# Kernel tuning notes

Measured on AMD Instinct MI355X. Metric: run time of the kernel, lower is better.

The kernel has to match this reference:

```python
import jax, jax.numpy as jnp
import numpy as np
from jax import lax

N_STEPS = 64  # fixed-step RK4 stands in for torchdiffeq's adaptive dopri5
INPUT_DIM = 64
HIDDEN_DIM = 256
BATCH = 262144


def setup_inputs() -> dict:
    key = jax.random.key(0)
    k_x, k_t, k_w1, k_b1, k_w2, k_b2 = jax.random.split(key, 6)
    x = jax.random.normal(k_x, (BATCH, INPUT_DIM), dtype=jnp.float32)
    t = jax.random.uniform(k_t, (1,), dtype=jnp.float32, minval=0.1, maxval=1.0)
    # torch Linear convention: y = x @ W.T + b
    s1 = 1.0 / np.sqrt(INPUT_DIM)
    s2 = 1.0 / np.sqrt(HIDDEN_DIM)
    W1 = jax.random.uniform(k_w1, (HIDDEN_DIM, INPUT_DIM), jnp.float32, -s1, s1)
    b1 = jax.random.uniform(k_b1, (HIDDEN_DIM,), jnp.float32, -s1, s1)
    W2 = jax.random.uniform(k_w2, (INPUT_DIM, HIDDEN_DIM), jnp.float32, -s2, s2)
    b2 = jax.random.uniform(k_b2, (INPUT_DIM,), jnp.float32, -s2, s2)
    return {"x": x, "t": t, "W1": W1, "b1": b1, "W2": W2, "b2": b2}


def reference(x, t, W1, b1, W2, b2):
    # ODE dynamics: f(y) = Linear2(ELU(Linear1(y))) -- autonomous (no t dependence)
    def f(y):
        h = jax.nn.elu(y @ W1.T + b1)  # [B, H]
        return h @ W2.T + b2           # [B, D]

    t0 = jnp.reshape(t, (-1,))[0]      # t.squeeze(); integrate over [0, t0]
    dt = t0 / N_STEPS

    def step(y, _):
        k1 = f(y)
        k2 = f(y + 0.5 * dt * k1)
        k3 = f(y + 0.5 * dt * k2)
        k4 = f(y + dt * k3)
        y_next = y + (dt / 6.0) * (k1 + 2.0 * k2 + 2.0 * k3 + k4)
        return y_next, None

    y_final, _ = lax.scan(step, x, None, length=N_STEPS)
    return y_final  # out[-1]: state at time t0
```

## Files before the change

### kernel.cpp

```cpp
#include <hip/hip_runtime.h>

#define NSTEP 64

typedef short bf8 __attribute__((ext_vector_type(8)));
typedef float f32x16 __attribute__((ext_vector_type(16)));
typedef float f32x4 __attribute__((ext_vector_type(4)));
typedef float f32x2 __attribute__((ext_vector_type(2)));
typedef unsigned int u32x4 __attribute__((ext_vector_type(4)));
typedef unsigned int u32x2 __attribute__((ext_vector_type(2)));

static __device__ __forceinline__ float asf(unsigned int u){ return __builtin_bit_cast(float, u); }
static __device__ __forceinline__ unsigned int asu(float f){ return __builtin_bit_cast(unsigned int, f); }

#if defined(__has_builtin)
#if __has_builtin(__builtin_amdgcn_cvt_pk_bf16_f32)
#define HAVE_CVT_PK_BF16 1
#endif
#endif
#ifdef HAVE_CVT_PK_BF16
typedef __bf16 bf16x2_t __attribute__((ext_vector_type(2)));
static __device__ __forceinline__ unsigned int pk(float a, float b){
  bf16x2_t r = __builtin_amdgcn_cvt_pk_bf16_f32(a, b);
  return __builtin_bit_cast(unsigned int, r);
}
#else
static __device__ __forceinline__ unsigned int pk(float a, float b){
  unsigned int ua = asu(a); unsigned int ub = asu(b);
  ua += 0x7FFFu + ((ua >> 16) & 1u);
  ub += 0x7FFFu + ((ub >> 16) & 1u);
  return (ua >> 16) | (ub & 0xFFFF0000u);
}
#endif

static __device__ __forceinline__ float bfr(float w){ return asf(pk(w, 0.0f) << 16); }

static __device__ __forceinline__ f32x2 pkfma(f32x2 a, f32x2 b, f32x2 c){
  return __builtin_elementwise_fma(a, b, c);
}

static __device__ __forceinline__ f32x2 pairof(const f32x16& v, int j){
  f32x2 r; r.x = v[2*j]; r.y = v[2*j+1]; return r;
}
static __device__ __forceinline__ void setpair(f32x16& v, int j, f32x2 p){
  v[2*j] = p.x; v[2*j+1] = p.y;
}

static __device__ __forceinline__ bf8 scale_bf8(bf8 w, float s){
  u32x4 u = __builtin_bit_cast(u32x4, w);
  u32x4 r;
  #pragma unroll
  for(int i=0;i<4;i++){
    float lo = asf(u[i] << 16) * s;
    float hi = asf(u[i] & 0xFFFF0000u) * s;
    r[i] = pk(lo, hi);
  }
  return __builtin_bit_cast(bf8, r);
}

#define MFMA16 __builtin_amdgcn_mfma_f32_16x16x32_bf16


#define ELU2(A, H0, H1) { \
  f32x2 q0; q0.x=A[0]; q0.y=A[1]; \
  f32x2 q1; q1.x=A[2]; q1.y=A[3]; \
  f32x2 m0 = __builtin_elementwise_max(q0, Z2); \
  f32x2 n0 = __builtin_elementwise_min(q0, Z2); \
  f32x2 m1 = __builtin_elementwise_max(q1, Z2); \
  f32x2 n1 = __builtin_elementwise_min(q1, Z2); \
  f32x2 e0; e0.x=__builtin_amdgcn_exp2f(n0.x); e0.y=__builtin_amdgcn_exp2f(n0.y); \
  f32x2 e1; e1.x=__builtin_amdgcn_exp2f(n1.x); e1.y=__builtin_amdgcn_exp2f(n1.y); \
  f32x2 h0 = pkfma(m0, LN22, e0); \
  f32x2 h1 = pkfma(m1, LN22, e1); \
  H0 = pk(h0.x, h0.y); H1 = pk(h1.x, h1.y); \
}

__global__ __launch_bounds__(128, 2) void ode_kernel(
    const void* __restrict__ xv,
    const void* __restrict__ tv,
    const void* __restrict__ W1v,
    const void* __restrict__ b1v,
    const void* __restrict__ W2v,
    const void* __restrict__ b2v,
    void* __restrict__ outv)
{
  __shared__ __align__(16) float b1s[256];
  __shared__ __align__(16) float b2s[64];
  __shared__ __align__(16) float xbuf[2][2][1024];

  const int tid = threadIdx.x;
  const int lid = tid & 63;
  const int wv  = tid >> 6;

  const unsigned int* w1u = (const unsigned int*)W1v;
  bool bad = false;
  #pragma unroll
  for(int i=0; i<2; i++){
    unsigned int d = w1u[i*64 + lid];
    unsigned int e0 = (d >> 7)  & 0xFFu;
    unsigned int e1 = (d >> 23) & 0xFFu;
    bad |= (e0 >= 125u) || (e1 >= 125u);
  }
  const bool f32in = (__ballot(bad) != 0ull);

  const float L2E = 1.4426950408889634f;

  if(f32in){
    #pragma unroll
    for(int i=0; i<2; i++) b1s[tid + i*128] = ((const float*)b1v)[tid + i*128] * L2E;
  } else {
    #pragma unroll
    for(int i=0; i<2; i++)
      b1s[tid + i*128] = asf((unsigned int)((const unsigned short*)b1v)[tid + i*128] << 16) * L2E;
  }
  if(tid < 64){
    float ssum = 0.0f;
    if(f32in){
      const float* W2 = (const float*)W2v + tid*256;
      #pragma unroll 4
      for(int k=0; k<64; k++){
        f32x4 w4 = *(const f32x4*)(W2 + k*4);
        ssum += bfr(w4[0]) + bfr(w4[1]) + bfr(w4[2]) + bfr(w4[3]);
      }
    } else {
      const unsigned short* W2 = (const unsigned short*)W2v + tid*256;
      for(int k=0; k<256; k++) ssum += asf((unsigned int)W2[k] << 16);
    }
    float bb = f32in ? ((const float*)b2v)[tid]
                     : asf((unsigned int)((const unsigned short*)b2v)[tid] << 16);
    b2s[tid] = (bb - ssum) * 0.5f;
  }
  __syncthreads();

  const int ln = lid & 15;
  const int g  = lid >> 4;
  const int g4 = g * 4;
  const int rr = blockIdx.x * 16 + ln;

  const float t  = f32in ? ((const float*)tv)[0]
                         : asf((unsigned int)((const unsigned short*)tv)[0] << 16);
  const float dt  = t / (float)NSTEP;
  const float hdt = 0.5f * dt;
  const float gg  = dt * (1.0f/6.0f);
  const f32x2 DT2  = {dt, dt};
  const f32x2 HDT2 = {hdt, hdt};
  const f32x2 TWO2 = {2.0f, 2.0f};
  const f32x2 G2   = {gg, gg};
  const f32x2 LN22 = {0.6931471805599453f, 0.6931471805599453f};
  const f32x2 Z2   = {0.0f, 0.0f};

  bf8 W1f[8][2];
  bf8 W2f[4][4];
  if(f32in){
    const float* W1 = (const float*)W1v;
    const float* W2 = (const float*)W2v;
    #pragma unroll
    for(int mtl=0; mtl<8; mtl++){
      #pragma unroll
      for(int ks=0; ks<2; ks++){
        const float* p = W1 + (wv*128 + mtl*16 + ln)*64 + ks*32 + g4;
        f32x4 a = *(const f32x4*)p;
        f32x4 b = *(const f32x4*)(p + 16);
        u32x4 u;
        u[0]=pk(a[0]*L2E, a[1]*L2E); u[1]=pk(a[2]*L2E, a[3]*L2E);
        u[2]=pk(b[0]*L2E, b[1]*L2E); u[3]=pk(b[2]*L2E, b[3]*L2E);
        W1f[mtl][ks] = __builtin_bit_cast(bf8, u);
      }
    }
    #pragma unroll
    for(int mt=0; mt<4; mt++){
      #pragma unroll
      for(int kt=0; kt<4; kt++){
        const float* p = W2 + (mt*16 + ln)*256 + wv*128 + kt*32 + g4;
        f32x4 a = *(const f32x4*)p;
        f32x4 b = *(const f32x4*)(p + 16);
        u32x4 u; u[0]=pk(a[0],a[1]); u[1]=pk(a[2],a[3]); u[2]=pk(b[0],b[1]); u[3]=pk(b[2],b[3]);
        W2f[mt][kt] = __builtin_bit_cast(bf8, u);
      }
    }
  } else {
    const unsigned short* W1 = (const unsigned short*)W1v;
    const unsigned short* W2 = (const unsigned short*)W2v;
    #pragma unroll
    for(int mtl=0; mtl<8; mtl++){
      #pragma unroll
      for(int ks=0; ks<2; ks++){
        const unsigned short* p = W1 + (wv*128 + mtl*16 + ln)*64 + ks*32 + g4;
        u32x2 lo = *(const u32x2*)p;
        u32x2 hi = *(const u32x2*)(p + 16);
        u32x4 u; u[0]=lo[0]; u[1]=lo[1]; u[2]=hi[0]; u[3]=hi[1];
        W1f[mtl][ks] = scale_bf8(__builtin_bit_cast(bf8, u), L2E);
      }
    }
    #pragma unroll
    for(int mt=0; mt<4; mt++){
      #pragma unroll
      for(int kt=0; kt<4; kt++){
        const unsigned short* p = W2 + (mt*16 + ln)*256 + wv*128 + kt*32 + g4;
        u32x2 lo = *(const u32x2*)p;
        u32x2 hi = *(const u32x2*)(p + 16);
        u32x4 u; u[0]=lo[0]; u[1]=lo[1]; u[2]=hi[0]; u[3]=hi[1];
        W2f[mt][kt] = __builtin_bit_cast(bf8, u);
      }
    }
  }

  f32x16 Y;
  if(f32in){
    const float* x = (const float*)xv;
    #pragma unroll
    for(int mt=0; mt<4; mt++){
      f32x4 v = *(const f32x4*)(x + rr*64 + mt*16 + g4);
      #pragma unroll
      for(int i=0;i<4;i++) Y[4*mt+i] = v[i];
    }
  } else {
    const unsigned short* x = (const unsigned short*)xv;
    #pragma unroll
    for(int mt=0; mt<4; mt++){
      u32x2 v = *(const u32x2*)(x + rr*64 + mt*16 + g4);
      Y[4*mt+0]=asf(v[0]<<16); Y[4*mt+1]=asf(v[0]&0xFFFF0000u);
      Y[4*mt+2]=asf(v[1]<<16); Y[4*mt+3]=asf(v[1]&0xFFFF0000u);
    }
  }

  f32x16 c2;
  #pragma unroll
  for(int i=0;i<16;i++) c2[i]=0.0f;

  #define CHUNK(KT) { \
    f32x4 a0 = *(const f32x4*)&b1s[wv*128 + (2*KT)*16 + g4]; \
    f32x4 a1 = *(const f32x4*)&b1s[wv*128 + (2*KT+1)*16 + g4]; \
    a0 = MFMA16(W1f[2*KT  ][0], zf0, a0, 0,0,0); \
    a0 = MFMA16(W1f[2*KT  ][1], zf1, a0, 0,0,0); \
    a1 = MFMA16(W1f[2*KT+1][0], zf0, a1, 0,0,0); \
    a1 = MFMA16(W1f[2*KT+1][1], zf1, a1, 0,0,0); \
    unsigned int H00,H01,H10,H11; \
    ELU2(a0, H00, H01) \
    ELU2(a1, H10, H11) \
    u32x4 hu; hu[0]=H00; hu[1]=H01; hu[2]=H10; hu[3]=H11; \
    bf8 hf = __builtin_bit_cast(bf8, hu); \
    p2[0] = MFMA16(W2f[0][KT], hf, p2[0], 0,0,0); \
    p2[1] = MFMA16(W2f[1][KT], hf, p2[1], 0,0,0); \
    p2[2] = MFMA16(W2f[2][KT], hf, p2[2], 0,0,0); \
    p2[3] = MFMA16(W2f[3][KT], hf, p2[3], 0,0,0); \
  }

  int par = 0;

  #pragma unroll 1
  for(int step=0; step<NSTEP; step++){
    f32x16 A;

    #pragma unroll
    for(int s=0; s<4; s++){
      unsigned int P[8];
      #pragma unroll
      for(int j=0; j<8; j++){
        f32x2 z;
        if(s == 0){ z = pairof(Y, j); }
        else {
          const f32x2 cc = (s==3) ? DT2 : HDT2;
          z = pkfma(cc, pairof(c2, j), pairof(Y, j));
        }
        P[j] = pk(z.x, z.y);
      }
      u32x4 z0u; z0u[0]=P[0]; z0u[1]=P[1]; z0u[2]=P[2]; z0u[3]=P[3];
      u32x4 z1u; z1u[0]=P[4]; z1u[1]=P[5]; z1u[2]=P[6]; z1u[3]=P[7];
      bf8 zf0 = __builtin_bit_cast(bf8, z0u);
      bf8 zf1 = __builtin_bit_cast(bf8, z1u);

      f32x4 p2[4];
      #pragma unroll
      for(int mt=0; mt<4; mt++) p2[mt] = *(const f32x4*)&b2s[mt*16 + g4];

      CHUNK(0) CHUNK(1) CHUNK(2) CHUNK(3)

      {
        float* my = &xbuf[par][wv][0];
        #pragma unroll
        for(int mt=0; mt<4; mt++)
          *(f32x4*)&my[(mt*64 + lid)*4] = p2[mt];
        __syncthreads();
        const float* prr = &xbuf[par][1-wv][0];
        #pragma unroll
        for(int mt=0; mt<4; mt++){
          f32x4 v = *(const f32x4*)&prr[(mt*64 + lid)*4];
          f32x2 s0; s0.x = p2[mt][0]+v[0]; s0.y = p2[mt][1]+v[1];
          f32x2 s1; s1.x = p2[mt][2]+v[2]; s1.y = p2[mt][3]+v[3];
          setpair(c2, 2*mt,   s0);
          setpair(c2, 2*mt+1, s1);
        }
        par ^= 1;
      }

      #pragma unroll
      for(int j=0;j<8;j++){
        if(s == 0)      setpair(A, j, pairof(c2, j));
        else if(s == 3) setpair(A, j, pairof(A, j) + pairof(c2, j));
        else            setpair(A, j, pkfma(TWO2, pairof(c2, j), pairof(A, j)));
      }
    }

    #pragma unroll
    for(int j=0;j<8;j++)
      setpair(Y, j, pkfma(G2, pairof(A, j), pairof(Y, j)));
  }

  if(wv == 0){
    if(f32in){
      float* out = (float*)outv;
      #pragma unroll
      for(int mt=0; mt<4; mt++){
        f32x4 v;
        #pragma unroll
        for(int i=0;i<4;i++) v[i] = Y[4*mt+i];
        *(f32x4*)(out + rr*64 + mt*16 + g4) = v;
      }
    } else {
      unsigned short* out = (unsigned short*)outv;
      #pragma unroll
      for(int mt=0; mt<4; mt++){
        u32x2 v;
        v[0] = pk(Y[4*mt+0], Y[4*mt+1]);
        v[1] = pk(Y[4*mt+2], Y[4*mt+3]);
        *(u32x2*)(out + rr*64 + mt*16 + g4) = v;
      }
    }
  }
}

extern "C" void kernel_launch(void* const* d_in, const int* in_sizes, int n_in,
                              void* d_out, int out_size, void* d_ws, size_t ws_size,
                              hipStream_t stream){
  hipLaunchKernelGGL(ode_kernel, dim3(16384), dim3(128), 0, stream,
                     d_in[0], d_in[1], d_in[2], d_in[3], d_in[4], d_in[5], d_out);
}
```

Measured before the change: 7.138 ms.

## Process two 16-row tiles per block to interleave independent MFMA chains

Each block now integrates 32 rows as two independent 16-row tiles whose MFMA/ELU chunks are interleaved, so each wave has two independent dependency chains to hide MFMA latency. The per-stage barrier and weight fragments are shared across both tiles. The grid is halved. Biases are hoisted from LDS into registers. This raises register pressure, so launch bounds drop to one block per SIMD-level hint, which risks lower occupancy or spills.

```diff
diff --git a/kernel.cpp b/kernel.cpp
--- a/kernel.cpp
+++ b/kernel.cpp
@@ -74,7 +74,50 @@
   H0 = pk(h0.x, h0.y); H1 = pk(h1.x, h1.y); \
 }
 
-__global__ __launch_bounds__(128, 2) void ode_kernel(
+#define PACKZ(S, Y_, C2_, ZF0, ZF1) \
+  bf8 ZF0, ZF1; { \
+    unsigned int P[8]; \
+    _Pragma("unroll") \
+    for(int j=0;j<8;j++){ \
+      f32x2 z; \
+      if((S)==0){ z = pairof(Y_, j); } \
+      else { const f32x2 cc = ((S)==3) ? DT2 : HDT2; \
+             z = pkfma(cc, pairof(C2_, j), pairof(Y_, j)); } \
+      P[j] = pk(z.x, z.y); \
+    } \
+    u32x4 u0; u0[0]=P[0]; u0[1]=P[1]; u0[2]=P[2]; u0[3]=P[3]; \
+    u32x4 u1; u1[0]=P[4]; u1[1]=P[5]; u1[2]=P[6]; u1[3]=P[7]; \
+    ZF0 = __builtin_bit_cast(bf8, u0); \
+    ZF1 = __builtin_bit_cast(bf8, u1); \
+  }
+
+#define CHUNK(KT, ZF0, ZF1, P2) { \
+  f32x4 a0 = b1r[2*(KT)]; \
+  f32x4 a1 = b1r[2*(KT)+1]; \
+  a0 = MFMA16(W1f[2*(KT)  ][0], ZF0, a0, 0,0,0); \
+  a0 = MFMA16(W1f[2*(KT)  ][1], ZF1, a0, 0,0,0); \
+  a1 = MFMA16(W1f[2*(KT)+1][0], ZF0, a1, 0,0,0); \
+  a1 = MFMA16(W1f[2*(KT)+1][1], ZF1, a1, 0,0,0); \
+  unsigned int H00,H01,H10,H11; \
+  ELU2(a0, H00, H01) \
+  ELU2(a1, H10, H11) \
+  u32x4 hu; hu[0]=H00; hu[1]=H01; hu[2]=H10; hu[3]=H11; \
+  bf8 hf = __builtin_bit_cast(bf8, hu); \
+  P2[0] = MFMA16(W2f[0][KT], hf, P2[0], 0,0,0); \
+  P2[1] = MFMA16(W2f[1][KT], hf, P2[1], 0,0,0); \
+  P2[2] = MFMA16(W2f[2][KT], hf, P2[2], 0,0,0); \
+  P2[3] = MFMA16(W2f[3][KT], hf, P2[3], 0,0,0); \
+}
+
+#define RKACC(S, A_, C2_) \
+  _Pragma("unroll") \
+  for(int j=0;j<8;j++){ \
+    if((S)==0)      setpair(A_, j, pairof(C2_, j)); \
+    else if((S)==3) setpair(A_, j, pairof(A_, j) + pairof(C2_, j)); \
+    else            setpair(A_, j, pkfma(TWO2, pairof(C2_, j), pairof(A_, j))); \
+  }
+
+__global__ __launch_bounds__(128, 1) void ode_kernel(
     const void* __restrict__ xv,
     const void* __restrict__ tv,
     const void* __restrict__ W1v,
@@ -85,7 +128,7 @@
 {
   __shared__ __align__(16) float b1s[256];
   __shared__ __align__(16) float b2s[64];
-  __shared__ __align__(16) float xbuf[2][2][1024];
+  __shared__ __align__(16) float xbuf[2][2][2][1024];
 
   const int tid = threadIdx.x;
   const int lid = tid & 63;
@@ -134,7 +177,8 @@
   const int ln = lid & 15;
   const int g  = lid >> 4;
   const int g4 = g * 4;
-  const int rr = blockIdx.x * 16 + ln;
+  const int rA = blockIdx.x * 32 + ln;
+  const int rB = rA + 16;
 
   const float t  = f32in ? ((const float*)tv)[0]
                          : asf((unsigned int)((const unsigned short*)tv)[0] << 16);
@@ -148,6 +192,13 @@
   const f32x2 LN22 = {0.6931471805599453f, 0.6931471805599453f};
   const f32x2 Z2   = {0.0f, 0.0f};
 
+  f32x4 b1r[8];
+  #pragma unroll
+  for(int tl=0; tl<8; tl++) b1r[tl] = *(const f32x4*)&b1s[wv*128 + tl*16 + g4];
+  f32x4 b2r[4];
+  #pragma unroll
+  for(int mt=0; mt<4; mt++) b2r[mt] = *(const f32x4*)&b2s[mt*16 + g4];
+
   bf8 W1f[8][2];
   bf8 W2f[4][4];
   if(f32in){
@@ -204,106 +255,89 @@
     }
   }
 
-  f32x16 Y;
+  f32x16 YA, YB;
   if(f32in){
     const float* x = (const float*)xv;
     #pragma unroll
     for(int mt=0; mt<4; mt++){
-      f32x4 v = *(const f32x4*)(x + rr*64 + mt*16 + g4);
-      #pragma unroll
-      for(int i=0;i<4;i++) Y[4*mt+i] = v[i];
+      f32x4 vA = *(const f32x4*)(x + rA*64 + mt*16 + g4);
+      f32x4 vB = *(const f32x4*)(x + rB*64 + mt*16 + g4);
+      #pragma unroll
+      for(int i=0;i<4;i++){ YA[4*mt+i] = vA[i]; YB[4*mt+i] = vB[i]; }
     }
   } else {
     const unsigned short* x = (const unsigned short*)xv;
     #pragma unroll
     for(int mt=0; mt<4; mt++){
-      u32x2 v = *(const u32x2*)(x + rr*64 + mt*16 + g4);
-      Y[4*mt+0]=asf(v[0]<<16); Y[4*mt+1]=asf(v[0]&0xFFFF0000u);
-      Y[4*mt+2]=asf(v[1]<<16); Y[4*mt+3]=asf(v[1]&0xFFFF0000u);
-    }
-  }
-
-  f32x16 c2;
-  #pragma unroll
-  for(int i=0;i<16;i++) c2[i]=0.0f;
-
-  #define CHUNK(KT) { \
-    f32x4 a0 = *(const f32x4*)&b1s[wv*128 + (2*KT)*16 + g4]; \
-    f32x4 a1 = *(const f32x4*)&b1s[wv*128 + (2*KT+1)*16 + g4]; \
-    a0 = MFMA16(W1f[2*KT  ][0], zf0, a0, 0,0,0); \
-    a0 = MFMA16(W1f[2*KT  ][1], zf1, a0, 0,0,0); \
-    a1 = MFMA16(W1f[2*KT+1][0], zf0, a1, 0,0,0); \
-    a1 = MFMA16(W1f[2*KT+1][1], zf1, a1, 0,0,0); \
-    unsigned int H00,H01,H10,H11; \
-    ELU2(a0, H00, H01) \
-    ELU2(a1, H10, H11) \
-    u32x4 hu; hu[0]=H00; hu[1]=H01; hu[2]=H10; hu[3]=H11; \
-    bf8 hf = __builtin_bit_cast(bf8, hu); \
-    p2[0] = MFMA16(W2f[0][KT], hf, p2[0], 0,0,0); \
-    p2[1] = MFMA16(W2f[1][KT], hf, p2[1], 0,0,0); \
-    p2[2] = MFMA16(W2f[2][KT], hf, p2[2], 0,0,0); \
-    p2[3] = MFMA16(W2f[3][KT], hf, p2[3], 0,0,0); \
-  }
+      u32x2 vA = *(const u32x2*)(x + rA*64 + mt*16 + g4);
+      u32x2 vB = *(const u32x2*)(x + rB*64 + mt*16 + g4);
+      YA[4*mt+0]=asf(vA[0]<<16); YA[4*mt+1]=asf(vA[0]&0xFFFF0000u);
+      YA[4*mt+2]=asf(vA[1]<<16); YA[4*mt+3]=asf(vA[1]&0xFFFF0000u);
+      YB[4*mt+0]=asf(vB[0]<<16); YB[4*mt+1]=asf(vB[0]&0xFFFF0000u);
+      YB[4*mt+2]=asf(vB[1]<<16); YB[4*mt+3]=asf(vB[1]&0xFFFF0000u);
+    }
+  }
+
+  f32x16 c2A, c2B;
+  #pragma unroll
+  for(int i=0;i<16;i++){ c2A[i]=0.0f; c2B[i]=0.0f; }
 
   int par = 0;
 
   #pragma unroll 1
   for(int step=0; step<NSTEP; step++){
-    f32x16 A;
+    f32x16 AA, AB;
 
     #pragma unroll
     for(int s=0; s<4; s++){
-      unsigned int P[8];
-      #pragma unroll
-      for(int j=0; j<8; j++){
-        f32x2 z;
-        if(s == 0){ z = pairof(Y, j); }
-        else {
-          const f32x2 cc = (s==3) ? DT2 : HDT2;
-          z = pkfma(cc, pairof(c2, j), pairof(Y, j));
-        }
-        P[j] = pk(z.x, z.y);
-      }
-      u32x4 z0u; z0u[0]=P[0]; z0u[1]=P[1]; z0u[2]=P[2]; z0u[3]=P[3];
-      u32x4 z1u; z1u[0]=P[4]; z1u[1]=P[5]; z1u[2]=P[6]; z1u[3]=P[7];
-      bf8 zf0 = __builtin_bit_cast(bf8, z0u);
-      bf8 zf1 = __builtin_bit_cast(bf8, z1u);
-
-      f32x4 p2[4];
-      #pragma unroll
-      for(int mt=0; mt<4; mt++) p2[mt] = *(const f32x4*)&b2s[mt*16 + g4];
-
-      CHUNK(0) CHUNK(1) CHUNK(2) CHUNK(3)
+      PACKZ(s, YA, c2A, zfA0, zfA1)
+      PACKZ(s, YB, c2B, zfB0, zfB1)
+
+      f32x4 p2A[4], p2B[4];
+      #pragma unroll
+      for(int mt=0; mt<4; mt++){ p2A[mt] = b2r[mt]; p2B[mt] = b2r[mt]; }
+
+      CHUNK(0, zfA0, zfA1, p2A) CHUNK(0, zfB0, zfB1, p2B)
+      CHUNK(1, zfA0, zfA1, p2A) CHUNK(1, zfB0, zfB1, p2B)
+      CHUNK(2, zfA0, zfA1, p2A) CHUNK(2, zfB0, zfB1, p2B)
+      CHUNK(3, zfA0, zfA1, p2A) CHUNK(3, zfB0, zfB1, p2B)
 
       {
-        float* my = &xbuf[par][wv][0];
-        #pragma unroll
-        for(int mt=0; mt<4; mt++)
-          *(f32x4*)&my[(mt*64 + lid)*4] = p2[mt];
-        __syncthreads();
-        const float* prr = &xbuf[par][1-wv][0];
+        float* myA = &xbuf[par][wv][0][0];
+        float* myB = &xbuf[par][wv][1][0];
         #pragma unroll
         for(int mt=0; mt<4; mt++){
-          f32x4 v = *(const f32x4*)&prr[(mt*64 + lid)*4];
-          f32x2 s0; s0.x = p2[mt][0]+v[0]; s0.y = p2[mt][1]+v[1];
-          f32x2 s1; s1.x = p2[mt][2]+v[2]; s1.y = p2[mt][3]+v[3];
-          setpair(c2, 2*mt,   s0);
-          setpair(c2, 2*mt+1, s1);
+          *(f32x4*)&myA[(mt*64 + lid)*4] = p2A[mt];
+          *(f32x4*)&myB[(mt*64 + lid)*4] = p2B[mt];
+        }
+        __syncthreads();
+        const float* prA = &xbuf[par][1-wv][0][0];
+        const float* prB = &xbuf[par][1-wv][1][0];
+        #pragma unroll
+        for(int mt=0; mt<4; mt++){
+          f32x4 vA = *(const f32x4*)&prA[(mt*64 + lid)*4];
+          f32x4 vB = *(const f32x4*)&prB[(mt*64 + lid)*4];
+          f32x2 a0; a0.x = p2A[mt][0]+vA[0]; a0.y = p2A[mt][1]+vA[1];
+          f32x2 a1; a1.x = p2A[mt][2]+vA[2]; a1.y = p2A[mt][3]+vA[3];
+          setpair(c2A, 2*mt,   a0);
+          setpair(c2A, 2*mt+1, a1);
+          f32x2 b0; b0.x = p2B[mt][0]+vB[0]; b0.y = p2B[mt][1]+vB[1];
+          f32x2 b1x; b1x.x = p2B[mt][2]+vB[2]; b1x.y = p2B[mt][3]+vB[3];
+          setpair(c2B, 2*mt,   b0);
+          setpair(c2B, 2*mt+1, b1x);
         }
         par ^= 1;
       }
 
-      #pragma unroll
-      for(int j=0;j<8;j++){
-        if(s == 0)      setpair(A, j, pairof(c2, j));
-        else if(s == 3) setpair(A, j, pairof(A, j) + pairof(c2, j));
-        else            setpair(A, j, pkfma(TWO2, pairof(c2, j), pairof(A, j)));
-      }
-    }
-
-    #pragma unroll
-    for(int j=0;j<8;j++)
-      setpair(Y, j, pkfma(G2, pairof(A, j), pairof(Y, j)));
+      RKACC(s, AA, c2A)
+      RKACC(s, AB, c2B)
+    }
+
+    #pragma unroll
+    for(int j=0;j<8;j++){
+      setpair(YA, j, pkfma(G2, pairof(AA, j), pairof(YA, j)));
+      setpair(YB, j, pkfma(G2, pairof(AB, j), pairof(YB, j)));
+    }
   }
 
   if(wv == 0){
@@ -311,19 +345,23 @@
       float* out = (float*)outv;
       #pragma unroll
       for(int mt=0; mt<4; mt++){
-        f32x4 v;
+        f32x4 vA, vB;
         #pragma unroll
-        for(int i=0;i<4;i++) v[i] = Y[4*mt+i];
-        *(f32x4*)(out + rr*64 + mt*16 + g4) = v;
+        for(int i=0;i<4;i++){ vA[i] = YA[4*mt+i]; vB[i] = YB[4*mt+i]; }
+        *(f32x4*)(out + rA*64 + mt*16 + g4) = vA;
+        *(f32x4*)(out + rB*64 + mt*16 + g4) = vB;
       }
     } else {
       unsigned short* out = (unsigned short*)outv;
       #pragma unroll
       for(int mt=0; mt<4; mt++){
-        u32x2 v;
-        v[0] = pk(Y[4*mt+0], Y[4*mt+1]);
-        v[1] = pk(Y[4*mt+2], Y[4*mt+3]);
-        *(u32x2*)(out + rr*64 + mt*16 + g4) = v;
+        u32x2 vA, vB;
+        vA[0] = pk(YA[4*mt+0], YA[4*mt+1]);
+        vA[1] = pk(YA[4*mt+2], YA[4*mt+3]);
+        vB[0] = pk(YB[4*mt+0], YB[4*mt+1]);
+        vB[1] = pk(YB[4*mt+2], YB[4*mt+3]);
+        *(u32x2*)(out + rA*64 + mt*16 + g4) = vA;
+        *(u32x2*)(out + rB*64 + mt*16 + g4) = vB;
       }
     }
   }
@@ -332,6 +370,6 @@
 extern "C" void kernel_launch(void* const* d_in, const int* in_sizes, int n_in,
                               void* d_out, int out_size, void* d_ws, size_t ws_size,
                               hipStream_t stream){
-  hipLaunchKernelGGL(ode_kernel, dim3(16384), dim3(128), 0, stream,
+  hipLaunchKernelGGL(ode_kernel, dim3(8192), dim3(128), 0, stream,
                      d_in[0], d_in[1], d_in[2], d_in[3], d_in[4], d_in[5], d_out);
 }
```

Result: slower. 8.584 ms (+20.3%).
